# Optimization experiments

Hardware: AMD Instinct MI355X
Metric: run time of the kernel (lower is better)

The kernel has to match this reference:

```python
import jax, jax.numpy as jnp
import numpy as np

N_NODES = 50000
N_EDGES = 800000
D = 128  # node_dim == edge_dim
NEG_SLOPE = 0.2


def setup_inputs() -> dict:
    key = jax.random.key(0)
    ks = jax.random.split(key, 16)
    w = lambda k, shp: (jax.random.normal(k, shp, dtype=jnp.float32) * 0.02)
    b = lambda: jnp.zeros((D,), dtype=jnp.float32)
    return {
        "V": jax.random.normal(ks[0], (N_NODES, D), dtype=jnp.float32),
        "E": jax.random.normal(ks[1], (N_EDGES, D), dtype=jnp.float32),
        "src": jax.random.randint(ks[2], (N_EDGES,), 0, N_NODES, dtype=jnp.int32),
        "dst": jax.random.randint(ks[3], (N_EDGES,), 0, N_NODES, dtype=jnp.int32),
        # NodePooling: two node_dim->node_dim linears
        "Wp1": w(ks[4], (D, D)), "bp1": b(),
        "Wp2": w(ks[5], (D, D)), "bp2": b(),
        # GenMessage.A: MLP with nb_mlp_layer=2 linears (edge_dim->edge_dim)
        "WA1": w(ks[6], (D, D)), "bA1": b(),
        "WA2": w(ks[7], (D, D)), "bA2": b(),
        # GenMessage.B (scale) and .C (shift): edge_dim->node_dim
        "WB": w(ks[8], (D, D)), "bB": b(),
        "WC": w(ks[9], (D, D)), "bC": b(),
    }


def reference(V, E, src, dst, Wp1, bp1, Wp2, bp2, WA1, bA1, WA2, bA2, WB, bB, WC, bC):
    lrelu = lambda x: jax.nn.leaky_relu(x, NEG_SLOPE)
    # V = act(V); G.ndata['V'] = pooling(V)
    Vp = lrelu(lrelu(V) @ Wp1.T + bp1) @ Wp2.T + bp2  # [N, D]
    # edge MLP on edge features (ReLU between linears, none after last)
    x = jax.nn.relu(E @ WA1.T + bA1) @ WA2.T + bA2    # [E, D]
    scale = jax.nn.sigmoid(x @ WB.T + bB)             # [E, D]
    shift = x @ WC.T + bC                             # [E, D]
    # per-edge gated message using gathered source node features
    msg = scale * Vp[src] + shift                     # [E, D]
    # scatter-sum into destination nodes (dgl.fn.sum)
    out = jax.ops.segment_sum(msg, dst, num_segments=N_NODES)  # [N, D]
    return out
```

## Files before the change

kernel.cpp:

```cpp
#include <hip/hip_runtime.h>
#include <hip/hip_bf16.h>

typedef __attribute__((ext_vector_type(8))) short bf16x8;
typedef __attribute__((ext_vector_type(4))) float f32x4;

#define DD 128

static __device__ __forceinline__ unsigned short f2bf(float f) {
    __bf16 h = (__bf16)f;
    return __builtin_bit_cast(unsigned short, h);
}
static __device__ __forceinline__ unsigned int pk2bf(float lo, float hi) {
    return ((unsigned int)f2bf(hi) << 16) | (unsigned int)f2bf(lo);
}
static __device__ __forceinline__ float bf2f(unsigned short h) {
    unsigned int u = ((unsigned int)h) << 16;
    return __builtin_bit_cast(float, u);
}

static __device__ __forceinline__ void lds_barrier() {
    asm volatile("s_waitcnt lgkmcnt(0)" ::: "memory");
    __builtin_amdgcn_s_barrier();
    asm volatile("" ::: "memory");
}

__global__ void k_convert(const float* __restrict__ w0, const float* __restrict__ w1,
                          const float* __restrict__ w2, const float* __restrict__ w3,
                          const float* __restrict__ w4, const float* __restrict__ w5,
                          unsigned short* __restrict__ wbf) {
    int i = blockIdx.x * blockDim.x + threadIdx.x;
    if (i >= 6 * 16384) return;
    int m = i >> 14, k = i & 16383;
    const float* s = (m == 0) ? w0 : (m == 1) ? w1 : (m == 2) ? w2 : (m == 3) ? w3
                     : (m == 4) ? w4 : w5;
    wbf[i] = f2bf(s[k]);
}

__global__ __launch_bounds__(256, 3) void k_nodes(
    const float* __restrict__ V, const unsigned short* __restrict__ wbf,
    const float* __restrict__ bp1, const float* __restrict__ bp2,
    unsigned short* __restrict__ Vp, int nN, int nTiles)
{
    const int lane = threadIdx.x & 63;
    const int wave = threadIdx.x >> 6;
    const int lr = lane & 15, lg = lane >> 4;

    bf16x8 B1[2][4], B2[2][4];
#pragma unroll
    for (int ct = 0; ct < 2; ++ct)
#pragma unroll
        for (int kk = 0; kk < 4; ++kk) {
            int j = wave * 32 + ct * 16 + lr;
            int k0 = kk * 32 + lg * 8;
            B1[ct][kk] = *(const bf16x8*)(wbf + 0 * 16384 + j * DD + k0);
            B2[ct][kk] = *(const bf16x8*)(wbf + 1 * 16384 + j * DD + k0);
        }
    float b1v[2], b2v[2];
#pragma unroll
    for (int ct = 0; ct < 2; ++ct) {
        int c = wave * 32 + ct * 16 + lr;
        b1v[ct] = bp1[c]; b2v[ct] = bp2[c];
    }
    __shared__ alignas(16) unsigned short xb[32][136];

    for (int t = blockIdx.x; t < nTiles; t += gridDim.x) {
        const int r0 = t * 32;
        bf16x8 A[2][4];
#pragma unroll
        for (int rg = 0; rg < 2; ++rg)
#pragma unroll
            for (int kk = 0; kk < 4; ++kk) {
                int row = r0 + rg * 16 + lr; if (row >= nN) row = nN - 1;
                const float4* p = (const float4*)(V + (size_t)row * DD + kk * 32 + lg * 8);
                float4 f0 = p[0], f1 = p[1];
                float v[8] = {f0.x, f0.y, f0.z, f0.w, f1.x, f1.y, f1.z, f1.w};
                bf16x8 a;
#pragma unroll
                for (int e = 0; e < 8; ++e) {
                    float x = v[e];
                    x = x > 0.f ? x : 0.2f * x;
                    a[e] = (short)f2bf(x);
                }
                A[rg][kk] = a;
            }
#pragma unroll
        for (int rg = 0; rg < 2; ++rg)
#pragma unroll
            for (int ct = 0; ct < 2; ++ct) {
                f32x4 acc = {0.f, 0.f, 0.f, 0.f};
#pragma unroll
                for (int kk = 0; kk < 4; ++kk)
                    acc = __builtin_amdgcn_mfma_f32_16x16x32_bf16(A[rg][kk], B1[ct][kk], acc, 0, 0, 0);
#pragma unroll
                for (int r = 0; r < 4; ++r) {
                    float x = acc[r] + b1v[ct];
                    x = x > 0.f ? x : 0.2f * x;
                    xb[rg * 16 + lg * 4 + r][wave * 32 + ct * 16 + lr] = f2bf(x);
                }
            }
        lds_barrier();
        bf16x8 A2[2][4];
#pragma unroll
        for (int rg = 0; rg < 2; ++rg)
#pragma unroll
            for (int kk = 0; kk < 4; ++kk)
                A2[rg][kk] = *(const bf16x8*)&xb[rg * 16 + lr][kk * 32 + lg * 8];
#pragma unroll
        for (int rg = 0; rg < 2; ++rg)
#pragma unroll
            for (int ct = 0; ct < 2; ++ct) {
                f32x4 acc = {0.f, 0.f, 0.f, 0.f};
#pragma unroll
                for (int kk = 0; kk < 4; ++kk)
                    acc = __builtin_amdgcn_mfma_f32_16x16x32_bf16(A2[rg][kk], B2[ct][kk], acc, 0, 0, 0);
#pragma unroll
                for (int r = 0; r < 4; ++r) {
                    int row = r0 + rg * 16 + lg * 4 + r;
                    if (row < nN)
                        Vp[(size_t)row * DD + wave * 32 + ct * 16 + lr] = f2bf(acc[r] + b2v[ct]);
                }
            }
        lds_barrier();
    }
}

__global__ __launch_bounds__(256, 2) void k_edges(
    const float* __restrict__ E, const int* __restrict__ src, const int* __restrict__ dst,
    const unsigned short* __restrict__ wbf,
    const float* __restrict__ bA1, const float* __restrict__ bA2,
    const float* __restrict__ bB, const float* __restrict__ bC,
    const unsigned short* __restrict__ Vp, float* __restrict__ out, int nE, int nTiles)
{
    const int lane = threadIdx.x & 63;
    const int wave = threadIdx.x >> 6;
    const int lr = lane & 15, lg = lane >> 4;
    const int srow = threadIdx.x >> 3;
    const int schunk = threadIdx.x & 7;

    bf16x8 B1[2][4], B2[2][4], B3[2][4], B4[2][4];
#pragma unroll
    for (int ct = 0; ct < 2; ++ct)
#pragma unroll
        for (int kk = 0; kk < 4; ++kk) {
            int j = wave * 32 + ct * 16 + lr;
            int k0 = kk * 32 + lg * 8;
            const unsigned short* p = wbf + 2 * 16384 + j * DD + k0;
            B1[ct][kk] = *(const bf16x8*)(p);
            B2[ct][kk] = *(const bf16x8*)(p + 16384);
            B3[ct][kk] = *(const bf16x8*)(p + 32768);
            B4[ct][kk] = *(const bf16x8*)(p + 49152);
        }
    float b1v[2], b2v[2], b3v[2], b4v[2];
#pragma unroll
    for (int ct = 0; ct < 2; ++ct) {
        int c = wave * 32 + ct * 16 + lr;
        b1v[ct] = bA1[c]; b2v[ct] = bA2[c]; b3v[ct] = bB[c]; b4v[ct] = bC[c];
    }
    __shared__ alignas(16) unsigned short xb[2][32][136];
    __shared__ alignas(16) unsigned short Eb[2][32][136];
    __shared__ alignas(8)  unsigned short gv[32][132];

    const int gstep = gridDim.x;
    int t = blockIdx.x;

    uint2 g0, g1, g2, g3;
    {
        int grow = t * 32 + srow; if (grow >= nE) grow = nE - 1;
        const uint2* vp2 = (const uint2*)(Vp + (size_t)src[grow] * DD);
        g0 = vp2[schunk]; g1 = vp2[schunk + 8]; g2 = vp2[schunk + 16]; g3 = vp2[schunk + 24];
    }
    int diR[8];
#pragma unroll
    for (int rg = 0; rg < 2; ++rg)
#pragma unroll
        for (int r = 0; r < 4; ++r) {
            int row = t * 32 + rg * 16 + lg * 4 + r;
            if (row >= nE) row = nE - 1;
            diR[rg * 4 + r] = dst[row];
        }
    float4 pf0, pf1, pf2, pf3;
    {
        int nrow = (t + gstep) * 32 + srow; if (nrow >= nE) nrow = nE - 1;
        const float4* np = (const float4*)(E + (size_t)nrow * DD + schunk * 16);
        pf0 = np[0]; pf1 = np[1]; pf2 = np[2]; pf3 = np[3];
    }
    {
        int row = t * 32 + srow; if (row >= nE) row = nE - 1;
        const float4* p = (const float4*)(E + (size_t)row * DD + schunk * 16);
        float4 f0 = p[0], f1 = p[1], f2 = p[2], f3 = p[3];
        uint4 w0 = make_uint4(pk2bf(f0.x, f0.y), pk2bf(f0.z, f0.w),
                              pk2bf(f1.x, f1.y), pk2bf(f1.z, f1.w));
        uint4 w1 = make_uint4(pk2bf(f2.x, f2.y), pk2bf(f2.z, f2.w),
                              pk2bf(f3.x, f3.y), pk2bf(f3.z, f3.w));
        uint4* wp = (uint4*)&Eb[0][srow][schunk * 16];
        wp[0] = w0; wp[1] = w1;
    }
    lds_barrier();
    int cur = 0;

    for (; t < nTiles; t += gstep) {
        const int r0 = t * 32;
        bf16x8 A[2][4];
#pragma unroll
        for (int rg = 0; rg < 2; ++rg)
#pragma unroll
            for (int kk = 0; kk < 4; ++kk)
                A[rg][kk] = *(const bf16x8*)&Eb[cur][rg * 16 + lr][kk * 32 + lg * 8];
#pragma unroll
        for (int rg = 0; rg < 2; ++rg)
#pragma unroll
            for (int ct = 0; ct < 2; ++ct) {
                f32x4 acc = {0.f, 0.f, 0.f, 0.f};
#pragma unroll
                for (int kk = 0; kk < 4; ++kk)
                    acc = __builtin_amdgcn_mfma_f32_16x16x32_bf16(A[rg][kk], B1[ct][kk], acc, 0, 0, 0);
#pragma unroll
                for (int r = 0; r < 4; ++r) {
                    float x = fmaxf(acc[r] + b1v[ct], 0.f);
                    xb[0][rg * 16 + lg * 4 + r][wave * 32 + ct * 16 + lr] = f2bf(x);
                }
            }
        lds_barrier();
        *(uint2*)&gv[srow][schunk * 4]      = g0;
        *(uint2*)&gv[srow][schunk * 4 + 32] = g1;
        *(uint2*)&gv[srow][schunk * 4 + 64] = g2;
        *(uint2*)&gv[srow][schunk * 4 + 96] = g3;
        {
            int ngrow = (t + gstep) * 32 + srow; if (ngrow >= nE) ngrow = nE - 1;
            const uint2* nvp2 = (const uint2*)(Vp + (size_t)src[ngrow] * DD);
            g0 = nvp2[schunk]; g1 = nvp2[schunk + 8]; g2 = nvp2[schunk + 16]; g3 = nvp2[schunk + 24];
        }
        float4 nf0, nf1, nf2, nf3;
        {
            int nrow = (t + 2 * gstep) * 32 + srow;
            if (nrow >= nE) nrow = nE - 1;
            const float4* np = (const float4*)(E + (size_t)nrow * DD + schunk * 16);
            nf0 = np[0]; nf1 = np[1]; nf2 = np[2]; nf3 = np[3];
        }
        int diF[8];
#pragma unroll
        for (int rg = 0; rg < 2; ++rg)
#pragma unroll
            for (int r = 0; r < 4; ++r) {
                int row = (t + gstep) * 32 + rg * 16 + lg * 4 + r;
                if (row >= nE) row = nE - 1;
                diF[rg * 4 + r] = dst[row];
            }
        bf16x8 A2[2][4];
#pragma unroll
        for (int rg = 0; rg < 2; ++rg)
#pragma unroll
            for (int kk = 0; kk < 4; ++kk)
                A2[rg][kk] = *(const bf16x8*)&xb[0][rg * 16 + lr][kk * 32 + lg * 8];
#pragma unroll
        for (int rg = 0; rg < 2; ++rg)
#pragma unroll
            for (int ct = 0; ct < 2; ++ct) {
                f32x4 acc = {0.f, 0.f, 0.f, 0.f};
#pragma unroll
                for (int kk = 0; kk < 4; ++kk)
                    acc = __builtin_amdgcn_mfma_f32_16x16x32_bf16(A2[rg][kk], B2[ct][kk], acc, 0, 0, 0);
#pragma unroll
                for (int r = 0; r < 4; ++r)
                    xb[1][rg * 16 + lg * 4 + r][wave * 32 + ct * 16 + lr] = f2bf(acc[r] + b2v[ct]);
            }
        lds_barrier();
        {
            uint4 w0 = make_uint4(pk2bf(pf0.x, pf0.y), pk2bf(pf0.z, pf0.w),
                                  pk2bf(pf1.x, pf1.y), pk2bf(pf1.z, pf1.w));
            uint4 w1 = make_uint4(pk2bf(pf2.x, pf2.y), pk2bf(pf2.z, pf2.w),
                                  pk2bf(pf3.x, pf3.y), pk2bf(pf3.z, pf3.w));
            uint4* wp = (uint4*)&Eb[cur ^ 1][srow][schunk * 16];
            wp[0] = w0; wp[1] = w1;
        }
        bf16x8 A3[2][4];
#pragma unroll
        for (int rg = 0; rg < 2; ++rg)
#pragma unroll
            for (int kk = 0; kk < 4; ++kk)
                A3[rg][kk] = *(const bf16x8*)&xb[1][rg * 16 + lr][kk * 32 + lg * 8];
#pragma unroll
        for (int rg = 0; rg < 2; ++rg)
#pragma unroll
            for (int ct = 0; ct < 2; ++ct) {
                f32x4 aB = {0.f, 0.f, 0.f, 0.f}, aC = {0.f, 0.f, 0.f, 0.f};
#pragma unroll
                for (int kk = 0; kk < 4; ++kk) {
                    aB = __builtin_amdgcn_mfma_f32_16x16x32_bf16(A3[rg][kk], B3[ct][kk], aB, 0, 0, 0);
                    aC = __builtin_amdgcn_mfma_f32_16x16x32_bf16(A3[rg][kk], B4[ct][kk], aC, 0, 0, 0);
                }
                const int col = wave * 32 + ct * 16 + lr;
#pragma unroll
                for (int r = 0; r < 4; ++r) {
                    int idx = rg * 4 + r;
                    bool valid = (r0 + rg * 16 + lg * 4 + r) < nE;
                    float e = __expf(-(aB[r] + b3v[ct]));
                    float sc = __builtin_amdgcn_rcpf(1.f + e);
                    float sh = aC[r] + b4v[ct];
                    float v = bf2f(gv[rg * 16 + lg * 4 + r][col]);
                    float msg = sc * v + sh;
                    if (valid)
                        unsafeAtomicAdd(out + (size_t)diR[idx] * DD + col, msg);
                }
            }
        lds_barrier();
        cur ^= 1;
        pf0 = nf0; pf1 = nf1; pf2 = nf2; pf3 = nf3;
#pragma unroll
        for (int i = 0; i < 8; ++i) diR[i] = diF[i];
    }
}

extern "C" void kernel_launch(void* const* d_in, const int* in_sizes, int n_in,
                              void* d_out, int out_size, void* d_ws, size_t ws_size,
                              hipStream_t stream) {
    const float* V   = (const float*)d_in[0];
    const float* E   = (const float*)d_in[1];
    const int*   src = (const int*)d_in[2];
    const int*   dst = (const int*)d_in[3];
    const float* Wp1 = (const float*)d_in[4];  const float* bp1 = (const float*)d_in[5];
    const float* Wp2 = (const float*)d_in[6];  const float* bp2 = (const float*)d_in[7];
    const float* WA1 = (const float*)d_in[8];  const float* bA1 = (const float*)d_in[9];
    const float* WA2 = (const float*)d_in[10]; const float* bA2 = (const float*)d_in[11];
    const float* WB  = (const float*)d_in[12]; const float* bB  = (const float*)d_in[13];
    const float* WC  = (const float*)d_in[14]; const float* bC  = (const float*)d_in[15];
    float* out = (float*)d_out;

    const int nN = in_sizes[0] / DD;
    const int nE = in_sizes[1] / DD;
    const int nTilesN = (nN + 31) / 32;
    const int nTilesE = (nE + 31) / 32;

    unsigned short* wbf = (unsigned short*)d_ws;
    unsigned short* Vp  = (unsigned short*)((char*)d_ws + 196608);

    hipMemsetAsync(d_out, 0, (size_t)out_size * sizeof(float), stream);
    k_convert<<<(6 * 16384 + 255) / 256, 256, 0, stream>>>(Wp1, Wp2, WA1, WA2, WB, WC, wbf);
    int gN = nTilesN < 768 ? nTilesN : 768;
    k_nodes<<<gN, 256, 0, stream>>>(V, wbf, bp1, bp2, Vp, nN, nTilesN);
    int gE = nTilesE < 512 ? nTilesE : 512;
    k_edges<<<gE, 256, 0, stream>>>(E, src, dst, wbf, bA1, bA2, bB, bC, Vp, out, nE, nTilesE);
}
```

Measured before the change: 385.0 us.

## Sort edges by destination and pre-reduce messages in LDS before atomics

Adds a counting sort of edges by destination (histogram, single-block scan, scatter permutation) and has the edge kernel walk edges in that sorted order. Messages for a 32-edge tile go into an LDS buffer, and each column is summed across runs of equal destination, so far fewer global float atomics are issued. The cost is three extra launches plus a memset, a serial single-block scan over the node counts, permuted (non-contiguous) reads of E rows, and extra LDS use per block. The new path only runs when the workspace is large enough to hold the counts and the permutation.

```diff
diff --git a/kernel.cpp b/kernel.cpp
--- a/kernel.cpp
+++ b/kernel.cpp
@@ -36,6 +36,47 @@
     wbf[i] = f2bf(s[k]);
 }
 
+__global__ __launch_bounds__(256) void k_hist(const int* __restrict__ dst,
+                                              int* __restrict__ counts, int nE) {
+    for (int e = blockIdx.x * blockDim.x + threadIdx.x; e < nE; e += gridDim.x * blockDim.x)
+        atomicAdd(&counts[dst[e]], 1);
+}
+
+__global__ __launch_bounds__(1024) void k_scan(const int* __restrict__ counts,
+                                               int* __restrict__ cursor, int nN) {
+    __shared__ int ps[1024];
+    const int tid = threadIdx.x;
+    const int chunk = (nN + 1023) / 1024;
+    const int base = tid * chunk;
+    int s = 0;
+    for (int i = 0; i < chunk; ++i) {
+        int idx = base + i;
+        s += (idx < nN) ? counts[idx] : 0;
+    }
+    ps[tid] = s;
+    __syncthreads();
+    for (int off = 1; off < 1024; off <<= 1) {
+        int add = (tid >= off) ? ps[tid - off] : 0;
+        __syncthreads();
+        ps[tid] += add;
+        __syncthreads();
+    }
+    int run = (tid > 0) ? ps[tid - 1] : 0;
+    for (int i = 0; i < chunk; ++i) {
+        int idx = base + i;
+        if (idx < nN) { cursor[idx] = run; run += counts[idx]; }
+    }
+}
+
+__global__ __launch_bounds__(256) void k_perm(const int* __restrict__ dst,
+                                              int* __restrict__ cursor,
+                                              int* __restrict__ perm, int nE) {
+    for (int e = blockIdx.x * blockDim.x + threadIdx.x; e < nE; e += gridDim.x * blockDim.x) {
+        int pos = atomicAdd(&cursor[dst[e]], 1);
+        perm[pos] = e;
+    }
+}
+
 __global__ __launch_bounds__(256, 3) void k_nodes(
     const float* __restrict__ V, const unsigned short* __restrict__ wbf,
     const float* __restrict__ bp1, const float* __restrict__ bp2,
@@ -126,6 +167,7 @@
 
 __global__ __launch_bounds__(256, 2) void k_edges(
     const float* __restrict__ E, const int* __restrict__ src, const int* __restrict__ dst,
+    const int* __restrict__ perm, int use_perm,
     const unsigned short* __restrict__ wbf,
     const float* __restrict__ bA1, const float* __restrict__ bA2,
     const float* __restrict__ bB, const float* __restrict__ bC,
@@ -159,34 +201,32 @@
     __shared__ alignas(16) unsigned short xb[2][32][136];
     __shared__ alignas(16) unsigned short Eb[2][32][136];
     __shared__ alignas(8)  unsigned short gv[32][132];
+    __shared__ alignas(16) float msgb[32][132];
+    __shared__ int dstb[33];
 
     const int gstep = gridDim.x;
     int t = blockIdx.x;
 
+    auto pidx = [&](int i) -> int {
+        if (i >= nE) i = nE - 1;
+        return use_perm ? perm[i] : i;
+    };
+
+    int pe_t = pidx(t * 32 + srow);
+    int pe1  = pidx((t + gstep) * 32 + srow);
     uint2 g0, g1, g2, g3;
     {
-        int grow = t * 32 + srow; if (grow >= nE) grow = nE - 1;
-        const uint2* vp2 = (const uint2*)(Vp + (size_t)src[grow] * DD);
+        const uint2* vp2 = (const uint2*)(Vp + (size_t)src[pe_t] * DD);
         g0 = vp2[schunk]; g1 = vp2[schunk + 8]; g2 = vp2[schunk + 16]; g3 = vp2[schunk + 24];
     }
-    int diR[8];
-#pragma unroll
-    for (int rg = 0; rg < 2; ++rg)
-#pragma unroll
-        for (int r = 0; r < 4; ++r) {
-            int row = t * 32 + rg * 16 + lg * 4 + r;
-            if (row >= nE) row = nE - 1;
-            diR[rg * 4 + r] = dst[row];
-        }
+    int pd = ((t * 32 + srow) < nE) ? dst[pe_t] : -1;
     float4 pf0, pf1, pf2, pf3;
     {
-        int nrow = (t + gstep) * 32 + srow; if (nrow >= nE) nrow = nE - 1;
-        const float4* np = (const float4*)(E + (size_t)nrow * DD + schunk * 16);
+        const float4* np = (const float4*)(E + (size_t)pe1 * DD + schunk * 16);
         pf0 = np[0]; pf1 = np[1]; pf2 = np[2]; pf3 = np[3];
     }
     {
-        int row = t * 32 + srow; if (row >= nE) row = nE - 1;
-        const float4* p = (const float4*)(E + (size_t)row * DD + schunk * 16);
+        const float4* p = (const float4*)(E + (size_t)pe_t * DD + schunk * 16);
         float4 f0 = p[0], f1 = p[1], f2 = p[2], f3 = p[3];
         uint4 w0 = make_uint4(pk2bf(f0.x, f0.y), pk2bf(f0.z, f0.w),
                               pk2bf(f1.x, f1.y), pk2bf(f1.z, f1.w));
@@ -199,7 +239,6 @@
     int cur = 0;
 
     for (; t < nTiles; t += gstep) {
-        const int r0 = t * 32;
         bf16x8 A[2][4];
 #pragma unroll
         for (int rg = 0; rg < 2; ++rg)
@@ -225,27 +264,19 @@
         *(uint2*)&gv[srow][schunk * 4 + 32] = g1;
         *(uint2*)&gv[srow][schunk * 4 + 64] = g2;
         *(uint2*)&gv[srow][schunk * 4 + 96] = g3;
-        {
-            int ngrow = (t + gstep) * 32 + srow; if (ngrow >= nE) ngrow = nE - 1;
-            const uint2* nvp2 = (const uint2*)(Vp + (size_t)src[ngrow] * DD);
-            g0 = nvp2[schunk]; g1 = nvp2[schunk + 8]; g2 = nvp2[schunk + 16]; g3 = nvp2[schunk + 24];
-        }
+        if (schunk == 0) dstb[srow] = pd;
+        int pe2 = pidx((t + 2 * gstep) * 32 + srow);
         float4 nf0, nf1, nf2, nf3;
         {
-            int nrow = (t + 2 * gstep) * 32 + srow;
-            if (nrow >= nE) nrow = nE - 1;
-            const float4* np = (const float4*)(E + (size_t)nrow * DD + schunk * 16);
+            const float4* np = (const float4*)(E + (size_t)pe2 * DD + schunk * 16);
             nf0 = np[0]; nf1 = np[1]; nf2 = np[2]; nf3 = np[3];
         }
-        int diF[8];
-#pragma unroll
-        for (int rg = 0; rg < 2; ++rg)
-#pragma unroll
-            for (int r = 0; r < 4; ++r) {
-                int row = (t + gstep) * 32 + rg * 16 + lg * 4 + r;
-                if (row >= nE) row = nE - 1;
-                diF[rg * 4 + r] = dst[row];
-            }
+        {
+            int sl = src[pe1];
+            const uint2* nvp2 = (const uint2*)(Vp + (size_t)sl * DD);
+            g0 = nvp2[schunk]; g1 = nvp2[schunk + 8]; g2 = nvp2[schunk + 16]; g3 = nvp2[schunk + 24];
+        }
+        int pdn = (((t + gstep) * 32 + srow) < nE) ? dst[pe1] : -1;
         bf16x8 A2[2][4];
 #pragma unroll
         for (int rg = 0; rg < 2; ++rg)
@@ -292,22 +323,33 @@
                 const int col = wave * 32 + ct * 16 + lr;
 #pragma unroll
                 for (int r = 0; r < 4; ++r) {
-                    int idx = rg * 4 + r;
-                    bool valid = (r0 + rg * 16 + lg * 4 + r) < nE;
                     float e = __expf(-(aB[r] + b3v[ct]));
                     float sc = __builtin_amdgcn_rcpf(1.f + e);
                     float sh = aC[r] + b4v[ct];
                     float v = bf2f(gv[rg * 16 + lg * 4 + r][col]);
-                    float msg = sc * v + sh;
-                    if (valid)
-                        unsafeAtomicAdd(out + (size_t)diR[idx] * DD + col, msg);
+                    msgb[rg * 16 + lg * 4 + r][col] = sc * v + sh;
                 }
             }
         lds_barrier();
+        {
+            const int col = threadIdx.x & 127;
+            const int half = threadIdx.x >> 7;
+            float acc = 0.f;
+#pragma unroll
+            for (int r = half * 16; r < half * 16 + 16; ++r) {
+                acc += msgb[r][col];
+                bool flush = (r == half * 16 + 15) || (dstb[r + 1] != dstb[r]);
+                if (flush) {
+                    int d = dstb[r];
+                    if (d >= 0)
+                        unsafeAtomicAdd(out + (size_t)d * DD + col, acc);
+                    acc = 0.f;
+                }
+            }
+        }
         cur ^= 1;
         pf0 = nf0; pf1 = nf1; pf2 = nf2; pf3 = nf3;
-#pragma unroll
-        for (int i = 0; i < 8; ++i) diR[i] = diF[i];
+        pe1 = pe2; pd = pdn;
     }
 }
 
@@ -331,13 +373,28 @@
     const int nTilesN = (nN + 31) / 32;
     const int nTilesE = (nE + 31) / 32;
 
-    unsigned short* wbf = (unsigned short*)d_ws;
-    unsigned short* Vp  = (unsigned short*)((char*)d_ws + 196608);
+    char* wsb = (char*)d_ws;
+    unsigned short* wbf = (unsigned short*)wsb;
+    unsigned short* Vp  = (unsigned short*)(wsb + 196608);
+    size_t off_counts = 196608 + (size_t)nN * 256;
+    int* counts = (int*)(wsb + off_counts);
+    int* cursor = (int*)(wsb + off_counts + (size_t)nN * 4);
+    int* perm   = (int*)(wsb + off_counts + (size_t)nN * 8);
+    size_t ws_need = off_counts + (size_t)nN * 8 + (size_t)nE * 4;
+    int use_perm = (ws_size >= ws_need) ? 1 : 0;
 
     hipMemsetAsync(d_out, 0, (size_t)out_size * sizeof(float), stream);
     k_convert<<<(6 * 16384 + 255) / 256, 256, 0, stream>>>(Wp1, Wp2, WA1, WA2, WB, WC, wbf);
     int gN = nTilesN < 768 ? nTilesN : 768;
     k_nodes<<<gN, 256, 0, stream>>>(V, wbf, bp1, bp2, Vp, nN, nTilesN);
+
+    if (use_perm) {
+        hipMemsetAsync(counts, 0, (size_t)nN * 4, stream);
+        k_hist<<<1024, 256, 0, stream>>>(dst, counts, nE);
+        k_scan<<<1, 1024, 0, stream>>>(counts, cursor, nN);
+        k_perm<<<1024, 256, 0, stream>>>(dst, cursor, perm, nE);
+    }
     int gE = nTilesE < 512 ? nTilesE : 512;
-    k_edges<<<gE, 256, 0, stream>>>(E, src, dst, wbf, bA1, bA2, bB, bC, Vp, out, nE, nTilesE);
-}
+    k_edges<<<gE, 256, 0, stream>>>(E, src, dst, perm, use_perm, wbf,
+                                    bA1, bA2, bB, bC, Vp, out, nE, nTilesE);
+}
```

Result: slower. 419.5 us (+9.0%).
